# Kernel tuning notes

Measured on AMD Instinct MI355X. Metric: run time of the kernel, lower is better.

## Reference

```python
import jax, jax.numpy as jnp
import numpy as np

B, T, H, W = 4, 8, 256, 256


def _shift(u, axis, d):
    """Value at index i comes from i+d along `axis`; zero (Dirichlet) boundary."""
    if d == 0:
        return u
    pad = [(0, 0)] * u.ndim
    sl = [slice(None)] * u.ndim
    if d > 0:
        sl[axis] = slice(d, None)
        pad[axis] = (0, d)
    else:
        sl[axis] = slice(None, d)
        pad[axis] = (-d, 0)
    return jnp.pad(u[tuple(sl)], pad)


def custom_sigmoid(x, mn, mx):
    # matches NLL.custom_sigmoid: (sigmoid(x) + min/(max-min)) * (max-min)
    return (jax.nn.sigmoid(x) + mn / (mx - mn)) * (mx - mn)


def setup_inputs() -> dict:
    key = jax.random.key(0)
    k1, k2 = jax.random.split(key)
    x = jax.random.normal(k1, (B, T, H, W), dtype=jnp.float32)
    conv_w = jax.random.normal(k2, (8 * T, T, 3, 3), dtype=jnp.float32) * 0.05
    return {"x": x, "conv_w": conv_w}


def reference(x, conv_w):
    Bn, Tn, Hn, Wn = x.shape
    dt = dx = dy = 1.0  # st_lag = [1,1,1]

    # Encoder: Conv2d(n_t -> 8*n_t, 3x3, padding=1, bias=False)
    theta = jax.lax.conv_general_dilated(
        x, conv_w, window_strides=(1, 1), padding="SAME",
        dimension_numbers=("NCHW", "OIHW", "NCHW"))

    # reshape_params: split 8*n_t channels into SPDE fields, bounded to valid ranges
    kappa = custom_sigmoid(theta[:, :Tn], 0.01, 1.0)          # damping
    m1 = theta[:, Tn:2 * Tn]                                   # advection x
    m2 = theta[:, 2 * Tn:3 * Tn]                               # advection y
    Hxx = custom_sigmoid(theta[:, 3 * Tn:4 * Tn], 0.01, 1.0)  # diffusion tensor
    Hxy = 0.1 * jnp.tanh(theta[:, 4 * Tn:5 * Tn])
    Hyx = 0.1 * jnp.tanh(theta[:, 5 * Tn:6 * Tn])
    Hyy = custom_sigmoid(theta[:, 6 * Tn:7 * Tn], 0.01, 1.0)
    tau = custom_sigmoid(theta[:, 7 * Tn:8 * Tn], 0.1, 10.0)   # noise scale

    # finite-difference stencils (zero Dirichlet boundary), vectorized over (B,T)
    def Dx(u):
        return (_shift(u, -1, 1) - _shift(u, -1, -1)) / (2 * dx)

    def Dy(u):
        return (_shift(u, -2, 1) - _shift(u, -2, -1)) / (2 * dy)

    def Dxx(u):
        return (_shift(u, -1, 1) + _shift(u, -1, -1) - 2 * u) / (dx * dx)

    def Dyy(u):
        return (_shift(u, -2, 1) + _shift(u, -2, -1) - 2 * u) / (dy * dy)

    def A(u):
        # advection-diffusion operator: kappa^2 u + m.grad u - div(H grad u)
        return ((kappa * kappa) * u + m1 * Dx(u) + m2 * Dy(u)
                - (Hxx * Dxx(u) + Hyy * Dyy(u) + (Hxy + Hyx) * Dx(Dy(u))))

    # pow=1 -> alpha=2 -> B = A^2 ; M_k = I + dt * B_k
    Mx = x + dt * A(A(x))                      # [B,T,H,W], M_k x_k for all k

    # Q = L^T D L with L block-bidiagonal (L[k,k]=M_k, L[k,k-1]=-I),
    # D_k = diag(dt / tau_k^2)  (inv_tau = sqrt(dt)/tau in create_Q)
    x_prev = jnp.concatenate([jnp.zeros_like(x[:, :1]), x[:, :-1]], axis=1)
    r = Mx - x_prev                            # r_k = M_k x_k - x_{k-1}
    D = dt / (tau * tau)

    xQx = jnp.sum(D * r * r)                   # quadratic form x^T Q x
    logdetD = jnp.sum(jnp.log(D))              # diagonal log-det contribution
    return 0.5 * (xQx - logdetD)
```

## Files before the change

kernel.cpp:

```cpp
#include <hip/hip_runtime.h>

#define IMG 65536

typedef _Float16 half8  __attribute__((ext_vector_type(8)));
typedef _Float16 half4v __attribute__((ext_vector_type(4)));
typedef _Float16 half2v __attribute__((ext_vector_type(2)));
typedef float    floatx4 __attribute__((ext_vector_type(4)));

__device__ __forceinline__ float sigm(float x){ return 1.0f/(1.0f + __expf(-x)); }
__device__ __forceinline__ float tanh_fast(float x){
    float t = __expf(2.0f*x);
    return 1.0f - 2.0f/(t + 1.0f);
}
__device__ __forceinline__ int swz(int px){ return px ^ ((px >> 3) & 7); }

__global__ void zero_out(float* out){ out[0] = 0.0f; }

__device__ __forceinline__ void row6(const float* __restrict__ u, int rb, int j0, float v[6]){
    const float4 c4 = *(const float4*)&u[rb + j0];
    v[1] = c4.x; v[2] = c4.y; v[3] = c4.z; v[4] = c4.w;
    v[0] = (j0 > 0)   ? u[rb + j0 - 1] : 0.0f;
    v[5] = (j0 < 252) ? u[rb + j0 + 4] : 0.0f;
}
__device__ __forceinline__ void zero6(float v[6]){ v[0]=v[1]=v[2]=v[3]=v[4]=v[5]=0.0f; }

__device__ __forceinline__ void stencil4(const float k2[4], const float m1[4],
    const float m2[4], const float hx[4], const float hs[4], const float hy[4],
    const float vc[6], const float vn[6], const float vs[6], float rp[4])
{
    #pragma unroll
    for (int p = 0; p < 4; ++p){
        float hxx = hx[p], hyy = hy[p];
        rp[p] = (k2[p] + 2.0f*(hxx + hyy))*vc[p+1]
              + (0.5f*m1[p] - hxx)*vc[p+2]
              - (0.5f*m1[p] + hxx)*vc[p]
              + (0.5f*m2[p] - hyy)*vn[p+1]
              - (0.5f*m2[p] + hyy)*vs[p+1]
              - 0.25f*hs[p]*(vn[p+2] - vs[p+2] - vn[p] + vs[p]);
    }
}

__global__ __launch_bounds__(512) void fused_all(
    const float* __restrict__ x, const float* __restrict__ w,
    float* __restrict__ out)
{
    __shared__ __align__(16) unsigned char smem[49536 + 81920];
    _Float16* xt  = (_Float16*)smem;
    _Float16* fl  = (_Float16*)(smem + 49536);
    float*    ys  = (float*)smem;
    float*    red = (float*)(smem + 21440);

    const int tid  = threadIdx.x;
    const int lane = tid & 63;
    const int wv   = tid >> 6;
    const int l16  = lane & 15;
    const int quad = lane >> 4;
    const int i0   = blockIdx.x << 3;
    const int b    = blockIdx.y >> 2;
    const int tp   = blockIdx.y & 3;

    {
        const int cp  = tid & 3;
        const int ccb = tid >> 2;
        const int pl  = ((b << 3) + (cp << 1)) << 16;
        #pragma unroll 2
        for (int rr = 0; rr < 12; ++rr){
            const int gi = i0 - 2 + rr;
            const bool rowok = (unsigned)gi < 256u;
            const int rowb = pl + (gi << 8);
            #pragma unroll
            for (int p = 0; p < 2; ++p){
                int cc = ccb + (p << 7);
                int gj = cc - 1;
                float v0 = 0.0f, v1 = 0.0f;
                if (rowok && (unsigned)gj < 256u){
                    v0 = x[rowb + gj];
                    v1 = x[rowb + gj + IMG];
                }
                half2v h; h[0] = (_Float16)v0; h[1] = (_Float16)v1;
                *(half2v*)&xt[(rr*258 + cc)*8 + (cp << 1)] = h;
            }
            if (tid < 8){
                int cc = 256 + (tid >> 2);
                int gj = cc - 1;
                float v0 = 0.0f, v1 = 0.0f;
                if (rowok && gj < 256){
                    v0 = x[rowb + gj];
                    v1 = x[rowb + gj + IMG];
                }
                half2v h; h[0] = (_Float16)v0; h[1] = (_Float16)v1;
                *(half2v*)&xt[(rr*258 + cc)*8 + (cp << 1)] = h;
            }
        }
    }

    half8 afr[3];
    int boff[3];
    {
        int oc = ((l16 & 7) << 3) + (tp << 1) + (l16 >> 3);
        #pragma unroll
        for (int s = 0; s < 3; ++s){
            int tap = s*4 + quad;
            half8 a;
            if (tap < 9){
                #pragma unroll
                for (int j = 0; j < 8; ++j)
                    a[j] = (_Float16)w[(oc*8 + j)*9 + tap];
                int dh = tap/3, dw = tap - dh*3;
                boff[s] = (dh*258 + dw)*8;
            } else {
                #pragma unroll
                for (int j = 0; j < 8; ++j) a[j] = (_Float16)0.0f;
                boff[s] = 0;
            }
            afr[s] = a;
        }
    }
    __syncthreads();

    float ldacc = 0.0f;
    const int tl_c  = quad >> 1;
    const int fhi   = quad & 1;
    #pragma unroll 2
    for (int it = 0; it < 20; ++it){
        const int g  = it*8 + wv;
        const int ry = g >> 4;
        const int jb = ((g & 15) << 4) + l16;
        const int base = (ry*258 + jb)*8;
        floatx4 acc = {0,0,0,0};
        #pragma unroll
        for (int s = 0; s < 3; ++s){
            half8 bf = *(const half8*)&xt[base + boff[s]];
            acc = __builtin_amdgcn_mfma_f32_16x16x32_f16(afr[s], bf, acc, 0, 0, 0);
        }
        const int flidx = ((((ry << 1) + tl_c) << 8) + swz(jb)) << 3;
        half4v v;
        if (fhi == 0){
            float s0 = 0.99f*sigm(acc[0]) + 0.01f;
            v[0] = (_Float16)(s0*s0);
            v[1] = (_Float16)acc[1];
            v[2] = (_Float16)acc[2];
            v[3] = (_Float16)(0.99f*sigm(acc[3]) + 0.01f);
            *(half4v*)&fl[flidx] = v;
        } else {
            float hs  = 0.1f*(tanh_fast(acc[0]) + tanh_fast(acc[1]));
            float hyy = 0.99f*sigm(acc[2]) + 0.01f;
            float tau = 9.9f*sigm(acc[3]) + 0.1f;
            v[0] = (_Float16)hs;
            v[1] = (_Float16)hyy;
            v[2] = (_Float16)(1.0f/(tau*tau));
            v[3] = (_Float16)0.0f;
            *(half4v*)&fl[flidx + 4] = v;
            if ((unsigned)(ry - 1) <= 7u)
                ldacc += __logf(tau);
        }
    }
    __syncthreads();

    if (tid < 40){
        int r2 = tid >> 1, side = tid & 1;
        ys[r2*268 + (side ? 260 : 3)] = 0.0f;
    }
    #pragma unroll
    for (int p = 0; p < 3; ++p){
        if (p == 2 && tid >= 256) break;
        const int task = p*512 + tid;
        const int cg   = task & 63;
        const int rowt = task >> 6;
        const int tl   = (rowt >= 10) ? 1 : 0;
        const int ry   = rowt - (tl ? 10 : 0);
        const int jc   = cg << 2;
        const int gi   = i0 - 1 + ry;
        float4 y4 = make_float4(0,0,0,0);
        if ((unsigned)gi < 256u){
            const int bt  = (b << 3) + (tp << 1) + tl;
            const int pix = (bt << 16) + (gi << 8) + jc;
            const int rb  = pix - jc;
            float vc[6], vn[6], vs[6];
            row6(x, rb, jc, vc);
            if (gi < 255) row6(x, rb + 256, jc, vn); else zero6(vn);
            if (gi > 0)   row6(x, rb - 256, jc, vs); else zero6(vs);
            float k2[4], m1[4], m2[4], hx[4], hsv[4], hy[4], yv[4];
            const int frow = (((ry << 1) + tl) << 8);
            #pragma unroll
            for (int q = 0; q < 4; ++q){
                half8 f8 = *(const half8*)&fl[(frow + swz(jc + q)) << 3];
                k2[q]=(float)f8[0]; m1[q]=(float)f8[1]; m2[q]=(float)f8[2];
                hx[q]=(float)f8[3]; hsv[q]=(float)f8[4]; hy[q]=(float)f8[5];
            }
            stencil4(k2, m1, m2, hx, hsv, hy, vc, vn, vs, yv);
            y4 = make_float4(yv[0], yv[1], yv[2], yv[3]);
        }
        *(float4*)&ys[(tl*10 + ry)*268 + 4 + jc] = y4;
    }
    __syncthreads();

    float local = 0.0f;
    #pragma unroll
    for (int p = 0; p < 2; ++p){
        const int task = p*512 + tid;
        const int cg   = task & 63;
        const int rowz = task >> 6;
        const int tl   = rowz >> 3;
        const int zr   = rowz & 7;
        const int jc   = cg << 2;
        const int gi   = i0 + zr;
        const int t    = (tp << 1) + tl;
        const int pix  = (((b << 3) + t) << 16) + (gi << 8) + jc;
        const int yb   = (tl*10 + zr + 1)*268 + 4 + jc;

        float vc[6], vn[6], vs[6];
        {
            float4 c4 = *(const float4*)&ys[yb];
            vc[1]=c4.x; vc[2]=c4.y; vc[3]=c4.z; vc[4]=c4.w;
            vc[0]=ys[yb-1]; vc[5]=ys[yb+4];
            float4 n4 = *(const float4*)&ys[yb+268];
            vn[1]=n4.x; vn[2]=n4.y; vn[3]=n4.z; vn[4]=n4.w;
            vn[0]=ys[yb+268-1]; vn[5]=ys[yb+268+4];
            float4 s4 = *(const float4*)&ys[yb-268];
            vs[1]=s4.x; vs[2]=s4.y; vs[3]=s4.z; vs[4]=s4.w;
            vs[0]=ys[yb-268-1]; vs[5]=ys[yb-268+4];
        }
        float k2[4], m1[4], m2[4], hx[4], hsv[4], hy[4], dv[4], zv[4];
        const int frow = ((((zr + 1) << 1) + tl) << 8);
        #pragma unroll
        for (int q = 0; q < 4; ++q){
            half8 f8 = *(const half8*)&fl[(frow + swz(jc + q)) << 3];
            k2[q]=(float)f8[0]; m1[q]=(float)f8[1]; m2[q]=(float)f8[2];
            hx[q]=(float)f8[3]; hsv[q]=(float)f8[4]; hy[q]=(float)f8[5];
            dv[q]=(float)f8[6];
        }
        stencil4(k2, m1, m2, hx, hsv, hy, vc, vn, vs, zv);

        float4 xc = *(const float4*)&x[pix];
        float4 xp = make_float4(0,0,0,0);
        if (t > 0) xp = *(const float4*)&x[pix - IMG];
        const float* xcp = (const float*)&xc;
        const float* xpp = (const float*)&xp;
        #pragma unroll
        for (int q = 0; q < 4; ++q){
            float r = xcp[q] + zv[q] - xpp[q];
            local += dv[q]*r*r;
        }
    }

    float v = 0.5f*local + ldacc;
    #pragma unroll
    for (int off = 1; off < 64; off <<= 1)
        v += __shfl_xor(v, off, 64);
    __syncthreads();
    if (lane == 0) red[wv] = v;
    __syncthreads();
    if (tid == 0){
        float s = 0.0f;
        #pragma unroll
        for (int k = 0; k < 8; ++k) s += red[k];
        atomicAdd(out, s);
    }
}

extern "C" void kernel_launch(void* const* d_in, const int* in_sizes, int n_in,
                              void* d_out, int out_size, void* d_ws, size_t ws_size,
                              hipStream_t stream)
{
    const float* x = (const float*)d_in[0];
    const float* w = (const float*)d_in[1];
    float* out = (float*)d_out;

    zero_out<<<1, 1, 0, stream>>>(out);
    fused_all<<<dim3(32, 16), 512, 0, stream>>>(x, w, out);
}
```

Baseline: 113.5 us.

## Split fused kernel into conv-fields pass and stencil pass via workspace

Breaks the single fused kernel into two launches. The first computes all 64 conv output channels per tile with four MFMA accumulators and writes the fp16 SPDE fields to a global workspace, with no halo recomputation. The second applies A twice using those fields read from global memory. This removes the redundant halo conv work and the large LDS footprint that limited occupancy, at the cost of a global round-trip for the field tensor (about 16 bytes per pixel) and an extra launch.

```diff
diff --git a/kernel.cpp b/kernel.cpp
--- a/kernel.cpp
+++ b/kernel.cpp
@@ -12,7 +12,6 @@
     float t = __expf(2.0f*x);
     return 1.0f - 2.0f/(t + 1.0f);
 }
-__device__ __forceinline__ int swz(int px){ return px ^ ((px >> 3) & 7); }
 
 __global__ void zero_out(float* out){ out[0] = 0.0f; }
 
@@ -40,32 +39,28 @@
     }
 }
 
-__global__ __launch_bounds__(512) void fused_all(
+__global__ __launch_bounds__(512) void conv_fields(
     const float* __restrict__ x, const float* __restrict__ w,
-    float* __restrict__ out)
-{
-    __shared__ __align__(16) unsigned char smem[49536 + 81920];
-    _Float16* xt  = (_Float16*)smem;
-    _Float16* fl  = (_Float16*)(smem + 49536);
-    float*    ys  = (float*)smem;
-    float*    red = (float*)(smem + 21440);
+    _Float16* __restrict__ fl, float* __restrict__ out)
+{
+    __shared__ _Float16 xt[6*258*8];
+    __shared__ float red[8];
 
     const int tid  = threadIdx.x;
     const int lane = tid & 63;
     const int wv   = tid >> 6;
     const int l16  = lane & 15;
     const int quad = lane >> 4;
-    const int i0   = blockIdx.x << 3;
-    const int b    = blockIdx.y >> 2;
-    const int tp   = blockIdx.y & 3;
+    const int i0   = blockIdx.x << 2;
+    const int b    = blockIdx.y;
 
     {
         const int cp  = tid & 3;
         const int ccb = tid >> 2;
         const int pl  = ((b << 3) + (cp << 1)) << 16;
-        #pragma unroll 2
-        for (int rr = 0; rr < 12; ++rr){
-            const int gi = i0 - 2 + rr;
+        #pragma unroll
+        for (int rr = 0; rr < 6; ++rr){
+            const int gi = i0 - 1 + rr;
             const bool rowok = (unsigned)gi < 256u;
             const int rowb = pl + (gi << 8);
             #pragma unroll
@@ -94,86 +89,113 @@
         }
     }
 
-    half8 afr[3];
+    half8 afr[4][3];
     int boff[3];
-    {
-        int oc = ((l16 & 7) << 3) + (tp << 1) + (l16 >> 3);
-        #pragma unroll
-        for (int s = 0; s < 3; ++s){
-            int tap = s*4 + quad;
+    #pragma unroll
+    for (int s = 0; s < 3; ++s){
+        const int tap = s*4 + quad;
+        const int tc  = (tap < 9) ? tap : 8;
+        const int dh  = tc/3, dw = tc - dh*3;
+        boff[s] = (dh*258 + dw)*8;
+        #pragma unroll
+        for (int g = 0; g < 4; ++g){
+            const int ocp = g*16 + l16;
+            const int oc  = ((ocp & 7) << 3) + (ocp >> 3);
             half8 a;
             if (tap < 9){
                 #pragma unroll
                 for (int j = 0; j < 8; ++j)
                     a[j] = (_Float16)w[(oc*8 + j)*9 + tap];
-                int dh = tap/3, dw = tap - dh*3;
-                boff[s] = (dh*258 + dw)*8;
             } else {
                 #pragma unroll
                 for (int j = 0; j < 8; ++j) a[j] = (_Float16)0.0f;
-                boff[s] = 0;
-            }
-            afr[s] = a;
+            }
+            afr[g][s] = a;
         }
     }
     __syncthreads();
 
     float ldacc = 0.0f;
-    const int tl_c  = quad >> 1;
-    const int fhi   = quad & 1;
+    const int thalf = quad >> 1;
+    const bool flo  = (quad & 1) == 0;
     #pragma unroll 2
-    for (int it = 0; it < 20; ++it){
-        const int g  = it*8 + wv;
-        const int ry = g >> 4;
-        const int jb = ((g & 15) << 4) + l16;
-        const int base = (ry*258 + jb)*8;
-        floatx4 acc = {0,0,0,0};
+    for (int it = 0; it < 8; ++it){
+        const int tile = it*8 + wv;
+        const int r    = tile >> 4;
+        const int jb   = ((tile & 15) << 4) + l16;
+        const int base = (r*258 + jb)*8;
+        floatx4 acc[4] = {{0,0,0,0},{0,0,0,0},{0,0,0,0},{0,0,0,0}};
         #pragma unroll
         for (int s = 0; s < 3; ++s){
             half8 bf = *(const half8*)&xt[base + boff[s]];
-            acc = __builtin_amdgcn_mfma_f32_16x16x32_f16(afr[s], bf, acc, 0, 0, 0);
-        }
-        const int flidx = ((((ry << 1) + tl_c) << 8) + swz(jb)) << 3;
-        half4v v;
-        if (fhi == 0){
-            float s0 = 0.99f*sigm(acc[0]) + 0.01f;
-            v[0] = (_Float16)(s0*s0);
-            v[1] = (_Float16)acc[1];
-            v[2] = (_Float16)acc[2];
-            v[3] = (_Float16)(0.99f*sigm(acc[3]) + 0.01f);
-            *(half4v*)&fl[flidx] = v;
-        } else {
-            float hs  = 0.1f*(tanh_fast(acc[0]) + tanh_fast(acc[1]));
-            float hyy = 0.99f*sigm(acc[2]) + 0.01f;
-            float tau = 9.9f*sigm(acc[3]) + 0.1f;
-            v[0] = (_Float16)hs;
-            v[1] = (_Float16)hyy;
-            v[2] = (_Float16)(1.0f/(tau*tau));
-            v[3] = (_Float16)0.0f;
-            *(half4v*)&fl[flidx + 4] = v;
-            if ((unsigned)(ry - 1) <= 7u)
+            acc[0] = __builtin_amdgcn_mfma_f32_16x16x32_f16(afr[0][s], bf, acc[0], 0, 0, 0);
+            acc[1] = __builtin_amdgcn_mfma_f32_16x16x32_f16(afr[1][s], bf, acc[1], 0, 0, 0);
+            acc[2] = __builtin_amdgcn_mfma_f32_16x16x32_f16(afr[2][s], bf, acc[2], 0, 0, 0);
+            acc[3] = __builtin_amdgcn_mfma_f32_16x16x32_f16(afr[3][s], bf, acc[3], 0, 0, 0);
+        }
+        const int gi = i0 + r;
+        #pragma unroll
+        for (int g = 0; g < 4; ++g){
+            const int t   = g*2 + thalf;
+            const int pix = ((((b << 3) + t) << 8) + gi << 8) + jb;
+            half4v v;
+            if (flo){
+                float s0 = 0.99f*sigm(acc[g][0]) + 0.01f;
+                v[0] = (_Float16)(s0*s0);
+                v[1] = (_Float16)acc[g][1];
+                v[2] = (_Float16)acc[g][2];
+                v[3] = (_Float16)(0.99f*sigm(acc[g][3]) + 0.01f);
+                *(half4v*)&fl[(pix << 3)] = v;
+            } else {
+                float hs  = 0.1f*(tanh_fast(acc[g][0]) + tanh_fast(acc[g][1]));
+                float hyy = 0.99f*sigm(acc[g][2]) + 0.01f;
+                float tau = 9.9f*sigm(acc[g][3]) + 0.1f;
+                v[0] = (_Float16)hs;
+                v[1] = (_Float16)hyy;
+                v[2] = (_Float16)(1.0f/(tau*tau));
+                v[3] = (_Float16)0.0f;
+                *(half4v*)&fl[(pix << 3) + 4] = v;
                 ldacc += __logf(tau);
-        }
-    }
-    __syncthreads();
-
-    if (tid < 40){
-        int r2 = tid >> 1, side = tid & 1;
-        ys[r2*268 + (side ? 260 : 3)] = 0.0f;
-    }
+            }
+        }
+    }
+
+    float v = ldacc;
+    #pragma unroll
+    for (int off = 1; off < 64; off <<= 1) v += __shfl_xor(v, off, 64);
+    if (lane == 0) red[wv] = v;
+    __syncthreads();
+    if (tid == 0){
+        float s = 0.0f;
+        #pragma unroll
+        for (int k = 0; k < 8; ++k) s += red[k];
+        atomicAdd(out, s);
+    }
+}
+
+__global__ __launch_bounds__(256) void fused_AA(
+    const float* __restrict__ x, const _Float16* __restrict__ fl,
+    float* __restrict__ out)
+{
+    __shared__ float ys[10*268];
+    __shared__ float red[4];
+
+    const int tid = threadIdx.x;
+    const int bt  = blockIdx.y;
+    const int t   = bt & 7;
+    const int i0  = blockIdx.x << 3;
+
+    if (tid < 20) ys[(tid >> 1)*268 + ((tid & 1) ? 260 : 3)] = 0.0f;
+
     #pragma unroll
     for (int p = 0; p < 3; ++p){
-        if (p == 2 && tid >= 256) break;
-        const int task = p*512 + tid;
-        const int cg   = task & 63;
-        const int rowt = task >> 6;
-        const int tl   = (rowt >= 10) ? 1 : 0;
-        const int ry   = rowt - (tl ? 10 : 0);
-        const int jc   = cg << 2;
-        const int gi   = i0 - 1 + ry;
+        if (p == 2 && tid >= 128) break;
+        const int task = p*256 + tid;
+        const int ry = task >> 6;
+        const int jc = (task & 63) << 2;
+        const int gi = i0 - 1 + ry;
         float4 y4 = make_float4(0,0,0,0);
         if ((unsigned)gi < 256u){
-            const int bt  = (b << 3) + (tp << 1) + tl;
             const int pix = (bt << 16) + (gi << 8) + jc;
             const int rb  = pix - jc;
             float vc[6], vn[6], vs[6];
@@ -181,33 +203,28 @@
             if (gi < 255) row6(x, rb + 256, jc, vn); else zero6(vn);
             if (gi > 0)   row6(x, rb - 256, jc, vs); else zero6(vs);
             float k2[4], m1[4], m2[4], hx[4], hsv[4], hy[4], yv[4];
-            const int frow = (((ry << 1) + tl) << 8);
             #pragma unroll
             for (int q = 0; q < 4; ++q){
-                half8 f8 = *(const half8*)&fl[(frow + swz(jc + q)) << 3];
+                half8 f8 = *(const half8*)&fl[(pix + q) << 3];
                 k2[q]=(float)f8[0]; m1[q]=(float)f8[1]; m2[q]=(float)f8[2];
                 hx[q]=(float)f8[3]; hsv[q]=(float)f8[4]; hy[q]=(float)f8[5];
             }
             stencil4(k2, m1, m2, hx, hsv, hy, vc, vn, vs, yv);
             y4 = make_float4(yv[0], yv[1], yv[2], yv[3]);
         }
-        *(float4*)&ys[(tl*10 + ry)*268 + 4 + jc] = y4;
+        *(float4*)&ys[ry*268 + 4 + jc] = y4;
     }
     __syncthreads();
 
     float local = 0.0f;
     #pragma unroll
     for (int p = 0; p < 2; ++p){
-        const int task = p*512 + tid;
-        const int cg   = task & 63;
-        const int rowz = task >> 6;
-        const int tl   = rowz >> 3;
-        const int zr   = rowz & 7;
-        const int jc   = cg << 2;
-        const int gi   = i0 + zr;
-        const int t    = (tp << 1) + tl;
-        const int pix  = (((b << 3) + t) << 16) + (gi << 8) + jc;
-        const int yb   = (tl*10 + zr + 1)*268 + 4 + jc;
+        const int task = p*256 + tid;
+        const int zr = task >> 6;
+        const int jc = (task & 63) << 2;
+        const int gi = i0 + zr;
+        const int pix = (bt << 16) + (gi << 8) + jc;
+        const int yb  = (zr + 1)*268 + 4 + jc;
 
         float vc[6], vn[6], vs[6];
         {
@@ -222,10 +239,9 @@
             vs[0]=ys[yb-268-1]; vs[5]=ys[yb-268+4];
         }
         float k2[4], m1[4], m2[4], hx[4], hsv[4], hy[4], dv[4], zv[4];
-        const int frow = ((((zr + 1) << 1) + tl) << 8);
         #pragma unroll
         for (int q = 0; q < 4; ++q){
-            half8 f8 = *(const half8*)&fl[(frow + swz(jc + q)) << 3];
+            half8 f8 = *(const half8*)&fl[(pix + q) << 3];
             k2[q]=(float)f8[0]; m1[q]=(float)f8[1]; m2[q]=(float)f8[2];
             hx[q]=(float)f8[3]; hsv[q]=(float)f8[4]; hy[q]=(float)f8[5];
             dv[q]=(float)f8[6];
@@ -244,19 +260,13 @@
         }
     }
 
-    float v = 0.5f*local + ldacc;
-    #pragma unroll
-    for (int off = 1; off < 64; off <<= 1)
-        v += __shfl_xor(v, off, 64);
-    __syncthreads();
-    if (lane == 0) red[wv] = v;
-    __syncthreads();
-    if (tid == 0){
-        float s = 0.0f;
-        #pragma unroll
-        for (int k = 0; k < 8; ++k) s += red[k];
-        atomicAdd(out, s);
-    }
+    float v = local;
+    #pragma unroll
+    for (int off = 1; off < 64; off <<= 1) v += __shfl_xor(v, off, 64);
+    if ((tid & 63) == 0) red[tid >> 6] = v;
+    __syncthreads();
+    if (tid == 0)
+        atomicAdd(out, 0.5f*(red[0] + red[1] + red[2] + red[3]));
 }
 
 extern "C" void kernel_launch(void* const* d_in, const int* in_sizes, int n_in,
@@ -266,7 +276,9 @@
     const float* x = (const float*)d_in[0];
     const float* w = (const float*)d_in[1];
     float* out = (float*)d_out;
+    _Float16* fl = (_Float16*)d_ws;
 
     zero_out<<<1, 1, 0, stream>>>(out);
-    fused_all<<<dim3(32, 16), 512, 0, stream>>>(x, w, out);
-}
+    conv_fields<<<dim3(64, 4), 512, 0, stream>>>(x, w, fl, out);
+    fused_AA<<<dim3(32, 32), 256, 0, stream>>>(x, fl, out);
+}
```

After: 116.5 us. 2.6% more time.
